# Optimization experiments

Hardware: AMD Instinct MI355X
Metric: run time of the kernel (lower is better)

## Reference

```python
import jax, jax.numpy as jnp
import numpy as np

HEADS = 16
DIM_HEAD = 64
LN_EPS = 1e-5


def rotate_half(t):
    # '... (j d) -> ... j d' with j=2, then cat(-x2, x1)
    d = t.shape[-1] // 2
    t1, t2 = t[..., :d], t[..., d:]
    return jnp.concatenate([-t2, t1], axis=-1)


def apply_rotary_pos_emb(t, pos):
    # t: (BT, h, L, dh); pos: (L, rotate_dim)
    rd = pos.shape[-1]
    pos = pos[None, None]  # (1, 1, L, rd)
    t_rot, t_pass = t[..., :rd], t[..., rd:]
    t_rot = t_rot * jnp.cos(pos) + rotate_half(t_rot) * jnp.sin(pos)
    return jnp.concatenate([t_rot, t_pass], axis=-1)


def setup_inputs() -> dict:
    key = jax.random.key(0)
    ks = jax.random.split(key, 4)
    B, T, L, D = 2, 8, 1024, 1024
    inner = HEADS * DIM_HEAD
    x = jax.random.normal(ks[0], (B, T * L, D), dtype=jnp.float32)
    gamma = jnp.ones((D,), jnp.float32)
    beta = jnp.zeros((D,), jnp.float32)
    W_qkv = jax.random.normal(ks[1], (D, 3 * inner), jnp.float32) * (D ** -0.5)
    b_qkv = jnp.zeros((3 * inner,), jnp.float32)
    W_out = jax.random.normal(ks[2], (inner, D), jnp.float32) * (inner ** -0.5)
    # standard GPT-NeoX-style rope angles for the spatial axis, rotate_dim=32
    rot_dim = 32
    inv_freq = 1.0 / (10000.0 ** (jnp.arange(0, rot_dim, 2, dtype=jnp.float32) / rot_dim))
    freqs = jnp.arange(L, dtype=jnp.float32)[:, None] * inv_freq[None, :]  # (L, 16)
    rotary_pos_emb = jnp.concatenate([freqs, freqs], axis=-1)  # (L, 32)
    return {"x": x, "gamma": gamma, "beta": beta, "W_qkv": W_qkv,
            "b_qkv": b_qkv, "W_out": W_out, "rotary_pos_emb": rotary_pos_emb,
            "T": T, "L": L}


def reference(x, gamma, beta, W_qkv, b_qkv, W_out, rotary_pos_emb, T, L):
    B, _, D = x.shape
    h, dh = HEADS, DIM_HEAD
    scale = dh ** -0.5
    # LayerNorm
    mean = jnp.mean(x, axis=-1, keepdims=True)
    var = jnp.mean(jnp.square(x - mean), axis=-1, keepdims=True)
    xn = (x - mean) * jax.lax.rsqrt(var + LN_EPS) * gamma + beta
    # (B, T*L, D) -> (B*T, L, D)
    xr = xn.reshape(B * T, L, D)
    qkv = xr @ W_qkv + b_qkv  # (BT, L, 3*h*dh)
    q, k, v = jnp.split(qkv, 3, axis=-1)
    def to_heads(t):
        return t.reshape(B * T, L, h, dh).transpose(0, 2, 1, 3)  # (BT, h, L, dh)
    q, k, v = map(to_heads, (q, k, v))
    q = apply_rotary_pos_emb(q, rotary_pos_emb)
    k = apply_rotary_pos_emb(k, rotary_pos_emb)
    sim = jnp.einsum('bhid,bhjd->bhij', q, k) * scale
    attn = jax.nn.softmax(sim.astype(jnp.float32), axis=-1).astype(q.dtype)
    out = jnp.einsum('bhij,bhjd->bhid', attn, v)  # (BT, h, L, dh)
    out = out.transpose(0, 2, 1, 3).reshape(B * T, L, h * dh)
    out = out @ W_out  # (BT, L, D)
    return out.reshape(B, T * L, D)
```

## Files before the change

### kernel.cpp

```cpp
#include <hip/hip_runtime.h>
#include <hip/hip_bf16.h>
#include <stdint.h>

typedef short bf16x8 __attribute__((ext_vector_type(8)));
typedef float f32x4  __attribute__((ext_vector_type(4)));
typedef unsigned short u16x4 __attribute__((ext_vector_type(4)));
typedef unsigned int   u32x2 __attribute__((ext_vector_type(2)));

#define DEV __device__ __forceinline__

DEV ushort f2bf(float f){
  unsigned u = __float_as_uint(f);
  u += 0x7FFFu + ((u >> 16) & 1u);
  return (ushort)(u >> 16);
}

DEV unsigned pack_bf16x2(float lo, float hi){
  __hip_bfloat162 r = __float22bfloat162_rn(float2{lo, hi});
  return *(unsigned*)&r;
}

DEV void async16(const void* g, void* l){
  __builtin_amdgcn_global_load_lds((const __attribute__((address_space(1))) void*)g,
                                   (__attribute__((address_space(3))) void*)l, 16, 0, 0);
}

__global__ __launch_bounds__(256) void preproc_kernel(
    const float* __restrict__ x, const float* __restrict__ gamma,
    const float* __restrict__ beta, ushort* __restrict__ xn,
    const float* __restrict__ Wqkv, ushort* __restrict__ Wqt,
    const float* __restrict__ Wout, ushort* __restrict__ Wot,
    const float* __restrict__ rope, float2* __restrict__ cst)
{
  __shared__ __align__(16) ushort tile[64][65];
  __shared__ float red[8];
  const int b = blockIdx.x, t = threadIdx.x;
  if (b < 16384) {
    const float4* xr = (const float4*)(x + (size_t)b * 1024);
    float4 v = xr[t];
    float s  = v.x + v.y + v.z + v.w;
    float s2 = v.x*v.x + v.y*v.y + v.z*v.z + v.w*v.w;
    #pragma unroll
    for (int o = 1; o < 64; o <<= 1) { s += __shfl_xor(s, o); s2 += __shfl_xor(s2, o); }
    int lane = t & 63, wv = t >> 6;
    if (lane == 0) { red[wv] = s; red[4 + wv] = s2; }
    __syncthreads();
    s  = red[0] + red[1] + red[2] + red[3];
    s2 = red[4] + red[5] + red[6] + red[7];
    float mean = s * (1.0f / 1024.0f);
    float var  = s2 * (1.0f / 1024.0f) - mean * mean;
    float rs = rsqrtf(var + 1e-5f);
    float4 g = ((const float4*)gamma)[t], bb = ((const float4*)beta)[t];
    u16x4 o4;
    o4[0] = f2bf((v.x - mean) * rs * g.x + bb.x);
    o4[1] = f2bf((v.y - mean) * rs * g.y + bb.y);
    o4[2] = f2bf((v.z - mean) * rs * g.z + bb.z);
    o4[3] = f2bf((v.w - mean) * rs * g.w + bb.w);
    ((u16x4*)(xn + (size_t)b * 1024))[t] = o4;
  } else if (b < 17408) {
    const float* A; ushort* At; int R, C, c0, r0;
    if (b < 17152) { int bb2 = b - 16384; A = Wqkv; At = Wqt; R = 1024; C = 3072;
                     c0 = (bb2 % 48) * 64; r0 = (bb2 / 48) * 64; }
    else           { int bb2 = b - 17152; A = Wout; At = Wot; R = 1024; C = 1024;
                     c0 = (bb2 % 16) * 64; r0 = (bb2 / 16) * 64; }
    int tx = t & 63, ty = t >> 6;
    #pragma unroll
    for (int i = 0; i < 64; i += 4)
      tile[ty + i][tx] = f2bf(A[(size_t)(r0 + ty + i) * C + c0 + tx]);
    __syncthreads();
    #pragma unroll
    for (int i = 0; i < 64; i += 4)
      At[(size_t)(c0 + ty + i) * R + r0 + tx] = tile[tx][ty + i];
  } else {
    int i = (b - 17408) * 256 + t;
    int l = i >> 4, d = i & 15;
    float p = rope[l * 32 + d];
    float s, c;
    sincosf(p, &s, &c);
    cst[i] = float2{c, s};
  }
}

template<bool OUT_BF16, bool HAS_BIAS, bool ROPE>
__global__ __launch_bounds__(512, 2) void gemm256_kernel(
    const ushort* __restrict__ A, const ushort* __restrict__ Bt,
    const float* __restrict__ bias, void* __restrict__ Cout,
    const float2* __restrict__ cst,
    int M, int Nrow, int K)
{
  __shared__ __align__(16) ushort As[2][2][256][32];
  __shared__ __align__(16) ushort Bs[2][2][256][32];
  const int tid = threadIdx.x, lane = tid & 63, w = tid >> 6;
  const int fr = lane & 15, fg = lane >> 4;
  const int wr = w >> 2, wc = w & 3;

  int i  = blockIdx.x & 255;
  int r  = blockIdx.x >> 8;
  int il = (i & 7) * 32 + (i >> 3);
  int bx = r * 4 + (il & 3);
  int by = il >> 2;
  const int aRow0 = by * 256, bCol0 = bx * 256;
  const size_t ldb = (size_t)K * 2;

  const int lrow = lane >> 2, lch = lane & 3;
  const int g0 = w * 2, g1 = w * 2 + 1;
  const int r0 = g0 * 16 + lrow, r1 = g1 * 16 + lrow;
  const int sc0 = ((lch ^ ((r0 & 3) ^ ((r0 >> 2) & 3))) << 4);
  const int sc1 = ((lch ^ ((r1 & 3) ^ ((r1 >> 2) & 3))) << 4);
  const char* Ab = (const char*)A + (size_t)aRow0 * ldb;
  const char* Bb = (const char*)Bt + (size_t)bCol0 * ldb;
  const size_t ga0 = (size_t)r0 * ldb, ga1 = (size_t)r1 * ldb;
  char* ldsA = (char*)&As[0][0][0][0];
  char* ldsB = (char*)&Bs[0][0][0][0];
  const int ld0 = g0 * 1024, ld1 = g1 * 1024;

  int rbA[8], rbB[4];
  #pragma unroll
  for (int mf = 0; mf < 8; ++mf) {
    int rr = wr * 128 + mf * 16 + fr;
    rbA[mf] = rr * 64 + ((fg ^ ((rr & 3) ^ ((rr >> 2) & 3))) << 4);
  }
  #pragma unroll
  for (int nf = 0; nf < 4; ++nf) {
    int rr = wc * 64 + nf * 16 + fr;
    rbB[nf] = rr * 64 + ((fg ^ ((rr & 3) ^ ((rr >> 2) & 3))) << 4);
  }

  f32x4 acc[8][4];
  f32x4 z = {0.f, 0.f, 0.f, 0.f};
  #pragma unroll
  for (int mf = 0; mf < 8; ++mf)
    #pragma unroll
    for (int nf = 0; nf < 4; ++nf) acc[mf][nf] = z;

  auto stage = [&](int buf, int kt, int kc) {
    const char* ak = Ab + (size_t)kt * 128 + kc * 64;
    const char* bk = Bb + (size_t)kt * 128 + kc * 64;
    int lo = buf * 32768 + kc * 16384;
    async16(ak + ga0 + sc0, ldsA + lo + ld0);
    async16(ak + ga1 + sc1, ldsA + lo + ld1);
    async16(bk + ga0 + sc0, ldsB + lo + ld0);
    async16(bk + ga1 + sc1, ldsB + lo + ld1);
  };

  stage(0, 0, 0);
  stage(0, 0, 1);
  asm volatile("s_waitcnt vmcnt(4)" ::: "memory");
  __builtin_amdgcn_s_barrier();

  const int nk = K >> 6;
  for (int kt = 0; kt < nk; ++kt) {
    int buf = kt & 1;
    bool pre = (kt + 1 < nk);
    #pragma unroll
    for (int kc = 0; kc < 2; ++kc) {
      const char* ab = ldsA + buf * 32768 + kc * 16384;
      const char* bb = ldsB + buf * 32768 + kc * 16384;
      bf16x8 a[8], b[4];
      #pragma unroll
      for (int mf = 0; mf < 8; ++mf) a[mf] = *(const bf16x8*)(ab + rbA[mf]);
      #pragma unroll
      for (int nf = 0; nf < 4; ++nf) b[nf] = *(const bf16x8*)(bb + rbB[nf]);
      if (pre) stage(buf ^ 1, kt + 1, kc);
      __builtin_amdgcn_s_setprio(1);
      #pragma unroll
      for (int mf = 0; mf < 8; ++mf)
        #pragma unroll
        for (int nf = 0; nf < 4; ++nf)
          acc[mf][nf] = __builtin_amdgcn_mfma_f32_16x16x32_bf16(a[mf], b[nf], acc[mf][nf], 0, 0, 0);
      __builtin_amdgcn_s_setprio(0);
      if (pre) { asm volatile("s_waitcnt vmcnt(4)" ::: "memory"); }
      else     { asm volatile("s_waitcnt vmcnt(0)" ::: "memory"); }
      __builtin_amdgcn_s_barrier();
    }
  }

  #pragma unroll
  for (int pr = 0; pr < 2; ++pr) {
    int nf0 = pr * 2, nf1 = nf0 + 1;
    int gc0 = bCol0 + wc * 64 + nf0 * 16 + fr;
    int gc1 = gc0 + 16;
    float bv0 = HAS_BIAS ? bias[gc0] : 0.0f;
    float bv1 = HAS_BIAS ? bias[gc1] : 0.0f;
    bool rot = ROPE && (pr == 0) && (gc0 < 2048);
    float qs = (ROPE && gc0 < 1024) ? 0.18033688f : 1.0f;
    #pragma unroll
    for (int mf = 0; mf < 8; ++mf) {
      int gr0 = aRow0 + wr * 128 + mf * 16 + fg * 4;
      #pragma unroll
      for (int rr2 = 0; rr2 < 4; ++rr2) {
        int gr = gr0 + rr2;
        float a = acc[mf][nf0][rr2] + bv0;
        float b = acc[mf][nf1][rr2] + bv1;
        if (rot) {
          int l = gr & 1023;
          float2 cp = cst[l * 16 + fr];
          float an = fmaf(a, cp.x, -b * cp.y);
          b = fmaf(b, cp.x, a * cp.y);
          a = an;
        }
        a *= qs; b *= qs;
        if (OUT_BF16) {
          ((ushort*)Cout)[(size_t)gr * Nrow + gc0] = f2bf(a);
          ((ushort*)Cout)[(size_t)gr * Nrow + gc1] = f2bf(b);
        } else {
          ((float*)Cout)[(size_t)gr * Nrow + gc0] = a;
          ((float*)Cout)[(size_t)gr * Nrow + gc1] = b;
        }
      }
    }
  }
}

__global__ __launch_bounds__(256) void vtrans_kernel(const ushort* __restrict__ qkv,
                                                     ushort* __restrict__ vT)
{
  __shared__ __align__(16) ushort tile[64][65];
  int bh = blockIdx.x & 255, lt = blockIdx.x >> 8;
  int bt = bh >> 4, h = bh & 15;
  int tx = threadIdx.x & 63, ty = threadIdx.x >> 6;
  const ushort* src = qkv + (size_t)(bt * 1024 + lt * 64) * 3072 + 2048 + h * 64;
  #pragma unroll
  for (int i = 0; i < 64; i += 4)
    tile[ty + i][tx] = src[(size_t)(ty + i) * 3072 + tx];
  __syncthreads();
  ushort* dst = vT + (size_t)bh * 64 * 1024 + lt * 64;
  #pragma unroll
  for (int i = 0; i < 64; i += 4)
    dst[(size_t)(ty + i) * 1024 + tx] = tile[tx][ty + i];
}

__global__ __launch_bounds__(512, 4) void attn_kernel(
    const ushort* __restrict__ qkv, const ushort* __restrict__ vT,
    ushort* __restrict__ aout)
{
  __shared__ __align__(16) ushort Ks[2][64 * 64];
  __shared__ __align__(16) ushort Vs[2][64 * 64];
  __shared__ __align__(16) ushort Ps[8][32 * 64];
  const int tid = threadIdx.x, lane = tid & 63, w = tid >> 6;
  const int fr = lane & 15, fg = lane >> 4;
  const int bh = blockIdx.x & 255, qt = blockIdx.x >> 8;
  const int bt = bh >> 4, h = bh & 15;
  const size_t ld = 3072;
  const ushort* qbase = qkv + (size_t)bt * 1024 * ld + h * 64;
  const ushort* kbase = qbase + 1024;
  const ushort* vtb = vT + (size_t)bh * 64 * 1024;
  const int srow = lane >> 3;
  const int scol = (((lane & 7) ^ srow) << 4);
  const int swz = (fr & 7) << 4;

  bf16x8 ones;
  #pragma unroll
  for (int j = 0; j < 8; ++j) ones[j] = (short)0x3F80;

  bf16x8 qfr[2][2];
  #pragma unroll
  for (int qf = 0; qf < 2; ++qf)
    #pragma unroll
    for (int kc = 0; kc < 2; ++kc) {
      int qrow = qt * 256 + w * 32 + qf * 16 + fr;
      qfr[qf][kc] = *(const bf16x8*)((const char*)(qbase + (size_t)qrow * ld) + kc * 64 + fg * 16);
    }

  f32x4 o[2][4], ls[2];
  f32x4 z = {0.f, 0.f, 0.f, 0.f};
  #pragma unroll
  for (int a = 0; a < 2; ++a) {
    ls[a] = z;
    #pragma unroll
    for (int b = 0; b < 4; ++b) o[a][b] = z;
  }
  float m_[2] = {-1e30f, -1e30f};

  auto stage = [&](int buf, int t) {
    async16((const char*)(kbase + (size_t)(t * 64 + w * 8 + srow) * ld) + scol,
            (char*)Ks[buf] + w * 1024);
    async16((const char*)(vtb + (size_t)(w * 8 + srow) * 1024) + t * 128 + scol,
            (char*)Vs[buf] + w * 1024);
  };

  stage(0, 0);
  __syncthreads();
  for (int t = 0; t < 16; ++t) {
    int cur = t & 1;
    if (t + 1 < 16) stage(cur ^ 1, t + 1);

    bf16x8 kf[4][2];
    #pragma unroll
    for (int kvf = 0; kvf < 4; ++kvf)
      #pragma unroll
      for (int kc = 0; kc < 2; ++kc)
        kf[kvf][kc] = *(const bf16x8*)((const char*)Ks[cur] + (kvf * 16 + fr) * 128 +
                                       ((kc * 64 + fg * 16) ^ swz));
    float alpha[2] = {1.0f, 1.0f};
    int   need[2];
    #pragma unroll
    for (int qf = 0; qf < 2; ++qf) {
      f32x4 st[4];
      #pragma unroll
      for (int kvf = 0; kvf < 4; ++kvf) st[kvf] = z;
      __builtin_amdgcn_s_setprio(1);
      #pragma unroll
      for (int kc = 0; kc < 2; ++kc)
        #pragma unroll
        for (int kvf = 0; kvf < 4; ++kvf)
          st[kvf] = __builtin_amdgcn_mfma_f32_16x16x32_bf16(kf[kvf][kc], qfr[qf][kc], st[kvf], 0, 0, 0);
      __builtin_amdgcn_s_setprio(0);
      float mx = -1e30f;
      #pragma unroll
      for (int kvf = 0; kvf < 4; ++kvf)
        #pragma unroll
        for (int r = 0; r < 4; ++r) mx = fmaxf(mx, st[kvf][r]);
      mx = fmaxf(mx, __shfl_xor(mx, 16));
      mx = fmaxf(mx, __shfl_xor(mx, 32));
      need[qf] = __any(mx > m_[qf] + 11.53f);
      if (need[qf]) {
        float mn = fmaxf(m_[qf], mx);
        alpha[qf] = __builtin_amdgcn_exp2f(m_[qf] - mn);
        m_[qf] = mn;
      }
      float mb = m_[qf];
      int qrow = qf * 16 + fr;
      #pragma unroll
      for (int kvf = 0; kvf < 4; ++kvf) {
        float p0 = __builtin_amdgcn_exp2f(st[kvf][0] - mb);
        float p1 = __builtin_amdgcn_exp2f(st[kvf][1] - mb);
        float p2 = __builtin_amdgcn_exp2f(st[kvf][2] - mb);
        float p3 = __builtin_amdgcn_exp2f(st[kvf][3] - mb);
        u32x2 u;
        u[0] = pack_bf16x2(p0, p1);
        u[1] = pack_bf16x2(p2, p3);
        *(u32x2*)((char*)Ps[w] + qrow * 128 + ((kvf * 32 + fg * 8) ^ swz)) = u;
      }
    }
    #pragma unroll
    for (int of = 0; of < 2; ++of) {
      if (need[of]) {
        float ar[4];
        #pragma unroll
        for (int r = 0; r < 4; ++r) ar[r] = __shfl(alpha[of], fg * 4 + r);
        #pragma unroll
        for (int cf = 0; cf < 4; ++cf)
          #pragma unroll
          for (int r = 0; r < 4; ++r) o[of][cf][r] *= ar[r];
        #pragma unroll
        for (int r = 0; r < 4; ++r) ls[of][r] *= ar[r];
      }
    }
    __builtin_amdgcn_s_setprio(1);
    #pragma unroll
    for (int kc4 = 0; kc4 < 2; ++kc4) {
      bf16x8 pa[2];
      #pragma unroll
      for (int of = 0; of < 2; ++of)
        pa[of] = *(const bf16x8*)((const char*)Ps[w] + (of * 16 + fr) * 128 +
                                  ((kc4 * 64 + fg * 16) ^ swz));
      #pragma unroll
      for (int cf = 0; cf < 4; ++cf) {
        bf16x8 vb = *(const bf16x8*)((const char*)Vs[cur] + (cf * 16 + fr) * 128 +
                                     ((kc4 * 64 + fg * 16) ^ swz));
        #pragma unroll
        for (int of = 0; of < 2; ++of)
          o[of][cf] = __builtin_amdgcn_mfma_f32_16x16x32_bf16(pa[of], vb, o[of][cf], 0, 0, 0);
      }
      #pragma unroll
      for (int of = 0; of < 2; ++of)
        ls[of] = __builtin_amdgcn_mfma_f32_16x16x32_bf16(pa[of], ones, ls[of], 0, 0, 0);
    }
    __builtin_amdgcn_s_setprio(0);
    __syncthreads();
  }
  #pragma unroll
  for (int of = 0; of < 2; ++of) {
    #pragma unroll
    for (int cf = 0; cf < 4; ++cf)
      #pragma unroll
      for (int r = 0; r < 4; ++r) {
        int grow_ = bt * 1024 + qt * 256 + w * 32 + of * 16 + fg * 4 + r;
        int gcol  = h * 64 + cf * 16 + fr;
        aout[(size_t)grow_ * 1024 + gcol] = f2bf(o[of][cf][r] / ls[of][r]);
      }
  }
}

extern "C" void kernel_launch(void* const* d_in, const int* in_sizes, int n_in,
                              void* d_out, int out_size, void* d_ws, size_t ws_size,
                              hipStream_t stream)
{
  const float* x     = (const float*)d_in[0];
  const float* gamma = (const float*)d_in[1];
  const float* beta  = (const float*)d_in[2];
  const float* Wqkv  = (const float*)d_in[3];
  const float* bqkv  = (const float*)d_in[4];
  const float* Wout  = (const float*)d_in[5];
  const float* rope  = (const float*)d_in[6];

  char* ws = (char*)d_ws;
  ushort* xn   = (ushort*)(ws + 0);
  ushort* qkvb = (ushort*)(ws + 33554432ULL);
  ushort* vT   = (ushort*)(ws + 134217728ULL);
  ushort* Wqt  = (ushort*)(ws + 167772160ULL);
  ushort* Wot  = (ushort*)(ws + 174063616ULL);
  float2* cst  = (float2*)(ws + 176160768ULL);
  ushort* aout = xn;

  preproc_kernel<<<17472, 256, 0, stream>>>(x, gamma, beta, xn,
                                            Wqkv, Wqt, Wout, Wot, rope, cst);
  gemm256_kernel<true, true, true><<<768, 512, 0, stream>>>(
      xn, Wqt, bqkv, (void*)qkvb, cst, 16384, 3072, 1024);
  vtrans_kernel<<<4096, 256, 0, stream>>>(qkvb, vT);
  attn_kernel<<<1024, 512, 0, stream>>>(qkvb, vT, aout);
  gemm256_kernel<false, false, false><<<256, 512, 0, stream>>>(
      aout, Wot, nullptr, d_out, nullptr, 16384, 1024, 1024);
}
```

Before: 323.3 us.

## Fuse V transpose into QKV GEMM epilogue and shrink attention blocks

The QKV GEMM epilogue now writes V columns directly into the transposed vT layout, which removes the separate vtrans kernel and its extra read and write of V. The attention kernel drops from 512 to 256 threads per block, with 128 query rows per block and twice as many blocks, and launch bounds change to allow 3 blocks per CU. Each wave now stages two K/V chunks. The transposed V stores from the GEMM epilogue are strided scalar writes, which may coalesce poorly, and smaller attention blocks reload each K/V tile for fewer query rows.

```diff
diff --git a/kernel.cpp b/kernel.cpp
--- a/kernel.cpp
+++ b/kernel.cpp
@@ -85,7 +85,7 @@
 __global__ __launch_bounds__(512, 2) void gemm256_kernel(
     const ushort* __restrict__ A, const ushort* __restrict__ Bt,
     const float* __restrict__ bias, void* __restrict__ Cout,
-    const float2* __restrict__ cst,
+    const float2* __restrict__ cst, ushort* __restrict__ vTo,
     int M, int Nrow, int K)
 {
   __shared__ __align__(16) ushort As[2][2][256][32];
@@ -183,6 +183,7 @@
     float bv0 = HAS_BIAS ? bias[gc0] : 0.0f;
     float bv1 = HAS_BIAS ? bias[gc1] : 0.0f;
     bool rot = ROPE && (pr == 0) && (gc0 < 2048);
+    bool isv = ROPE && (gc0 >= 2048);
     float qs = (ROPE && gc0 < 1024) ? 0.18033688f : 1.0f;
     #pragma unroll
     for (int mf = 0; mf < 8; ++mf) {
@@ -200,7 +201,13 @@
           a = an;
         }
         a *= qs; b *= qs;
-        if (OUT_BF16) {
+        if (isv) {
+          int d0 = gc0 - 2048;
+          int bhv = ((gr >> 10) << 4) + (d0 >> 6);
+          size_t vb = (size_t)bhv * 65536 + (size_t)(d0 & 63) * 1024 + (gr & 1023);
+          vTo[vb]             = f2bf(a);
+          vTo[vb + 16 * 1024] = f2bf(b);
+        } else if (OUT_BF16) {
           ((ushort*)Cout)[(size_t)gr * Nrow + gc0] = f2bf(a);
           ((ushort*)Cout)[(size_t)gr * Nrow + gc1] = f2bf(b);
         } else {
@@ -212,31 +219,13 @@
   }
 }
 
-__global__ __launch_bounds__(256) void vtrans_kernel(const ushort* __restrict__ qkv,
-                                                     ushort* __restrict__ vT)
-{
-  __shared__ __align__(16) ushort tile[64][65];
-  int bh = blockIdx.x & 255, lt = blockIdx.x >> 8;
-  int bt = bh >> 4, h = bh & 15;
-  int tx = threadIdx.x & 63, ty = threadIdx.x >> 6;
-  const ushort* src = qkv + (size_t)(bt * 1024 + lt * 64) * 3072 + 2048 + h * 64;
-  #pragma unroll
-  for (int i = 0; i < 64; i += 4)
-    tile[ty + i][tx] = src[(size_t)(ty + i) * 3072 + tx];
-  __syncthreads();
-  ushort* dst = vT + (size_t)bh * 64 * 1024 + lt * 64;
-  #pragma unroll
-  for (int i = 0; i < 64; i += 4)
-    dst[(size_t)(ty + i) * 1024 + tx] = tile[tx][ty + i];
-}
-
-__global__ __launch_bounds__(512, 4) void attn_kernel(
+__global__ __launch_bounds__(256, 3) void attn_kernel(
     const ushort* __restrict__ qkv, const ushort* __restrict__ vT,
     ushort* __restrict__ aout)
 {
   __shared__ __align__(16) ushort Ks[2][64 * 64];
   __shared__ __align__(16) ushort Vs[2][64 * 64];
-  __shared__ __align__(16) ushort Ps[8][32 * 64];
+  __shared__ __align__(16) ushort Ps[4][32 * 64];
   const int tid = threadIdx.x, lane = tid & 63, w = tid >> 6;
   const int fr = lane & 15, fg = lane >> 4;
   const int bh = blockIdx.x & 255, qt = blockIdx.x >> 8;
@@ -258,7 +247,7 @@
   for (int qf = 0; qf < 2; ++qf)
     #pragma unroll
     for (int kc = 0; kc < 2; ++kc) {
-      int qrow = qt * 256 + w * 32 + qf * 16 + fr;
+      int qrow = qt * 128 + w * 32 + qf * 16 + fr;
       qfr[qf][kc] = *(const bf16x8*)((const char*)(qbase + (size_t)qrow * ld) + kc * 64 + fg * 16);
     }
 
@@ -273,10 +262,14 @@
   float m_[2] = {-1e30f, -1e30f};
 
   auto stage = [&](int buf, int t) {
-    async16((const char*)(kbase + (size_t)(t * 64 + w * 8 + srow) * ld) + scol,
-            (char*)Ks[buf] + w * 1024);
-    async16((const char*)(vtb + (size_t)(w * 8 + srow) * 1024) + t * 128 + scol,
-            (char*)Vs[buf] + w * 1024);
+    #pragma unroll
+    for (int i = 0; i < 2; ++i) {
+      int ch = w * 2 + i;
+      async16((const char*)(kbase + (size_t)(t * 64 + ch * 8 + srow) * ld) + scol,
+              (char*)Ks[buf] + ch * 1024);
+      async16((const char*)(vtb + (size_t)(ch * 8 + srow) * 1024) + t * 128 + scol,
+              (char*)Vs[buf] + ch * 1024);
+    }
   };
 
   stage(0, 0);
@@ -376,7 +369,7 @@
     for (int cf = 0; cf < 4; ++cf)
       #pragma unroll
       for (int r = 0; r < 4; ++r) {
-        int grow_ = bt * 1024 + qt * 256 + w * 32 + of * 16 + fg * 4 + r;
+        int grow_ = bt * 1024 + qt * 128 + w * 32 + of * 16 + fg * 4 + r;
         int gcol  = h * 64 + cf * 16 + fr;
         aout[(size_t)grow_ * 1024 + gcol] = f2bf(o[of][cf][r] / ls[of][r]);
       }
@@ -407,9 +400,8 @@
   preproc_kernel<<<17472, 256, 0, stream>>>(x, gamma, beta, xn,
                                             Wqkv, Wqt, Wout, Wot, rope, cst);
   gemm256_kernel<true, true, true><<<768, 512, 0, stream>>>(
-      xn, Wqt, bqkv, (void*)qkvb, cst, 16384, 3072, 1024);
-  vtrans_kernel<<<4096, 256, 0, stream>>>(qkvb, vT);
-  attn_kernel<<<1024, 512, 0, stream>>>(qkvb, vT, aout);
+      xn, Wqt, bqkv, (void*)qkvb, cst, vT, 16384, 3072, 1024);
+  attn_kernel<<<2048, 256, 0, stream>>>(qkvb, vT, aout);
   gemm256_kernel<false, false, false><<<256, 512, 0, stream>>>(
-      aout, Wot, nullptr, d_out, nullptr, 16384, 1024, 1024);
-}
+      aout, Wot, nullptr, d_out, nullptr, nullptr, 16384, 1024, 1024);
+}
```

After: 329.1 us. Within noise of the previous version (+1.8%).
